# Kernel tuning notes

Hardware: AMD Instinct MI355X
Metric: run time of the kernel (lower is better)

## Reference

```python
import jax, jax.numpy as jnp
import numpy as np

T, B, I, H = 100, 64, 256, 512


def setup_inputs() -> dict:
    key = jax.random.key(0)
    ks = jax.random.split(key, 7)
    # torch kaiming_uniform_(a=sqrt(5)) + fan_in bias init -> uniform(-1/sqrt(fan_in), 1/sqrt(fan_in))
    b_ih = 1.0 / np.sqrt(I)
    b_hh = 1.0 / np.sqrt(H)
    return {
        "input": jax.random.normal(ks[0], (T, B, I), jnp.float32),
        "initial_h": jax.random.normal(ks[1], (B, H), jnp.float32),
        "initial_c": jax.random.normal(ks[2], (B, H), jnp.float32),
        "weight_ih": jax.random.uniform(ks[3], (4 * H, I), jnp.float32, -b_ih, b_ih),
        "weight_hh": jax.random.uniform(ks[4], (4 * H, H), jnp.float32, -b_hh, b_hh),
        "bias_ih": jax.random.uniform(ks[5], (4 * H,), jnp.float32, -b_ih, b_ih),
        "bias_hh": jax.random.uniform(ks[6], (4 * H,), jnp.float32, -b_hh, b_hh),
    }


def reference(input, initial_h, initial_c, weight_ih, weight_hh, bias_ih, bias_hh):
    Bsz, Isz = input.shape[1], input.shape[2]
    Hs = initial_h.shape[1]

    def step(carry, x_t):
        hx, cx, ev_ih, ev_hh, ev_b = carry
        # standard LSTM gates, torch gate order: i, f, g, o
        gates = x_t @ weight_ih.T + hx @ weight_hh.T + bias_ih + bias_hh  # [B,4H]
        i_g, f_g, g_g, o_g = jnp.split(gates, 4, axis=1)
        i = jax.nn.sigmoid(i_g)
        f = jax.nn.sigmoid(f_g)
        g = jnp.tanh(g_g)
        o = jax.nn.sigmoid(o_g)
        cy = f * cx + i * g
        hy = o * jnp.tanh(cy)
        # e-prop instantaneous derivatives of c_t wrt the i/f/g pre-activations
        d_i = g * i * (1.0 - i)          # [B,H]
        d_f = cx * f * (1.0 - f)
        d_g = i * (1.0 - g * g)
        d = jnp.concatenate([d_i, d_f, d_g], axis=1)[:, :, None]  # [B,3H,1]
        f3 = jnp.tile(f, (1, 3))[:, :, None]                      # [B,3H,1]
        # eligibility-trace recursion: ev_t = f_t * ev_{t-1} + d_t (outer) input
        ev_ih = f3 * ev_ih + d * x_t[:, None, :]   # [B,3H,I]
        ev_hh = f3 * ev_hh + d * hx[:, None, :]    # [B,3H,H]
        ev_b = f3 * ev_b + d                       # [B,3H,1]
        return (hy, cy, ev_ih, ev_hh, ev_b), hy

    ev_ih0 = jnp.zeros((Bsz, 3 * Hs, Isz), input.dtype)
    ev_hh0 = jnp.zeros((Bsz, 3 * Hs, Hs), input.dtype)
    ev_b0 = jnp.zeros((Bsz, 3 * Hs, 1), input.dtype)
    (hx, cx, ev_ih, ev_hh, ev_b), outputs = jax.lax.scan(
        step, (initial_h, initial_c, ev_ih0, ev_hh0, ev_b0), input
    )
    return outputs, cx, ev_ih, ev_hh, ev_b
```

## Files before the change

### kernel.cpp

```cpp
#include <hip/hip_runtime.h>
#include <math.h>

#define TT 100
#define BB 64
#define II 256
#define HH 512
#define G4H 2048
#define G3H 1536

#define OFF_GT    0
#define OFF_HBUF  13107200
#define OFF_FBUF  16416768
#define OFF_DBUF  19693568
#define OFF_CT    29523968
#define OFF_XT    29556736
#define OFF_WIHT  31195136
#define OFF_WHHT  31719424

#define O_OUT   0
#define O_CX    3276800
#define O_EVIH  3309568
#define O_EVHH  28475392
#define O_EVB   78807040

__global__ __launch_bounds__(256) void tp64(const float* __restrict__ src,
                                            float* __restrict__ dst,
                                            int R, int C,
                                            long sstride, long dstride) {
  __shared__ float tile[64][65];
  src += (long)blockIdx.z * sstride;
  dst += (long)blockIdx.z * dstride;
  int r0 = blockIdx.y * 64, c0 = blockIdx.x * 64;
  int tx = threadIdx.x & 15, tq = threadIdx.x >> 4;
#pragma unroll
  for (int p = 0; p < 4; ++p) {
    int rl = p * 16 + tq;
    float4 v = *(const float4*)(src + (long)(r0 + rl) * C + c0 + tx * 4);
    tile[rl][tx * 4 + 0] = v.x; tile[rl][tx * 4 + 1] = v.y;
    tile[rl][tx * 4 + 2] = v.z; tile[rl][tx * 4 + 3] = v.w;
  }
  __syncthreads();
#pragma unroll
  for (int p = 0; p < 4; ++p) {
    int cl = p * 16 + tq;
    float4 v;
    v.x = tile[tx * 4 + 0][cl]; v.y = tile[tx * 4 + 1][cl];
    v.z = tile[tx * 4 + 2][cl]; v.w = tile[tx * 4 + 3][cl];
    *(float4*)(dst + (long)(c0 + cl) * R + r0 + tx * 4) = v;
  }
}

__global__ __launch_bounds__(256) void make_whhg(const float* __restrict__ WhhT,
                                                 float* __restrict__ WhhG) {
  int gid = blockIdx.x * 256 + threadIdx.x;
  int k = gid >> 11, j = gid & 2047;
  float v = WhhT[gid];
  WhhG[(long)k * G4H + ((j & 511) << 2) + (j >> 9)] = v;
}

template <int BK, int KTILES, bool BIAS, bool ZSHIFT>
__global__ __launch_bounds__(256) void gemm_tn(
    const float* __restrict__ A, long batchA, int lda,
    const float* __restrict__ Z, long batchZ, int ldz,
    const float* __restrict__ Z0, long batchZ0,
    float* __restrict__ C, long batchC, int ldc,
    const float* __restrict__ bia, const float* __restrict__ bib) {
  __shared__ float As[BK][64];
  __shared__ float Zs[BK][64];
  int tid = threadIdx.x;
  int tn = tid & 15, tm = tid >> 4;
  int m0 = blockIdx.x * 64, n0 = blockIdx.y * 64;
  long bz = blockIdx.z;
  const float* Ab = A + bz * batchA + m0;
  const float* Zb = Z + bz * batchZ + n0;
  const float* Z0b = ZSHIFT ? (Z0 + bz * batchZ0 + n0) : nullptr;
  float acc[4][4] = {};
  for (int kt = 0; kt < KTILES; ++kt) {
    int k0 = kt * BK;
#pragma unroll
    for (int p = tid; p < BK * 64; p += 256) {
      int r = p >> 6, c = p & 63;
      int k = k0 + r;
      As[r][c] = Ab[(long)k * lda + c];
      const float* zr;
      if (ZSHIFT)
        zr = (k == 0) ? Z0b : (Zb + (long)(k - 1) * ldz);
      else
        zr = Zb + (long)k * ldz;
      Zs[r][c] = zr[c];
    }
    __syncthreads();
#pragma unroll 4
    for (int kk = 0; kk < BK; ++kk) {
      float4 a = *(const float4*)&As[kk][tm * 4];
      float4 z = *(const float4*)&Zs[kk][tn * 4];
      float av[4] = {a.x, a.y, a.z, a.w};
      float zv[4] = {z.x, z.y, z.z, z.w};
#pragma unroll
      for (int q = 0; q < 4; ++q)
#pragma unroll
        for (int r = 0; r < 4; ++r)
          acc[q][r] = fmaf(av[q], zv[r], acc[q][r]);
    }
    __syncthreads();
  }
  float* Cb = C + bz * batchC + n0 + tn * 4;
#pragma unroll
  for (int q = 0; q < 4; ++q) {
    int m = m0 + tm * 4 + q;
    float bv = BIAS ? (bia[m] + bib[m]) : 0.f;
    float4 v;
    v.x = acc[q][0] + bv; v.y = acc[q][1] + bv;
    v.z = acc[q][2] + bv; v.w = acc[q][3] + bv;
    *(float4*)(Cb + (long)m * ldc) = v;
  }
}

__global__ __launch_bounds__(512) void lstm_step2(const float* __restrict__ G_T,
                                                  const float* __restrict__ WhhG,
                                                  float* __restrict__ Hbuf,
                                                  float* __restrict__ cT,
                                                  float* __restrict__ Fbuf,
                                                  float* __restrict__ Dbuf,
                                                  int t) {
  __shared__ float red[2][4][4][64];
  int tid = threadIdx.x;
  int lane = tid & 63;
  int wave = __builtin_amdgcn_readfirstlane(tid >> 6);
  int hl = wave & 1, kp = wave >> 1;
  int hh = blockIdx.x * 2 + hl;
  float a0 = 0.f, a1 = 0.f, a2 = 0.f, a3 = 0.f;
  const float* hp = Hbuf + (long)t * (HH * BB) + kp * 128 * BB + lane;
  const float* wp = WhhG + (long)(kp * 128) * G4H + hh * 4;
#pragma unroll 4
  for (int k = 0; k < 128; ++k) {
    float h = hp[(long)k * BB];
    float4 w = *(const float4*)(wp + (long)k * G4H);
    a0 = fmaf(w.x, h, a0);
    a1 = fmaf(w.y, h, a1);
    a2 = fmaf(w.z, h, a2);
    a3 = fmaf(w.w, h, a3);
  }
  red[hl][kp][0][lane] = a0;
  red[hl][kp][1][lane] = a1;
  red[hl][kp][2][lane] = a2;
  red[hl][kp][3][lane] = a3;
  __syncthreads();
  if (tid < 128) {
    int b = tid & 63, h2 = tid >> 6;
    int hhx = blockIdx.x * 2 + h2;
    const float* gp = G_T + (long)t * (G4H * BB) + hhx * BB + b;
    float g[4];
#pragma unroll
    for (int q = 0; q < 4; ++q)
      g[q] = gp[(long)q * (HH * BB)] + red[h2][0][q][b] + red[h2][1][q][b] +
             red[h2][2][q][b] + red[h2][3][q][b];
    float ig = 1.f / (1.f + expf(-g[0]));
    float fg = 1.f / (1.f + expf(-g[1]));
    float gg = tanhf(g[2]);
    float og = 1.f / (1.f + expf(-g[3]));
    int idx = hhx * BB + b;
    float co = cT[idx];
    float cy = fg * co + ig * gg;
    cT[idx] = cy;
    Hbuf[(long)(t + 1) * (HH * BB) + idx] = og * tanhf(cy);
    Fbuf[(long)t * (HH * BB) + idx] = fg;
    float* dp = Dbuf + (long)t * (G3H * BB) + idx;
    dp[0] = gg * ig * (1.f - ig);
    dp[HH * BB] = co * fg * (1.f - fg);
    dp[2 * HH * BB] = ig * (1.f - gg * gg);
  }
}

__global__ __launch_bounds__(256) void suffix_scale(float* __restrict__ Dbuf,
                                                    const float* __restrict__ Fbuf,
                                                    float* __restrict__ evb) {
  int g = blockIdx.x * 256 + threadIdx.x;
  int b = g & 63, hh = g >> 6;
  float P = 1.f, e0 = 0.f, e1 = 0.f, e2 = 0.f;
#pragma unroll 2
  for (int t = TT - 1; t >= 0; --t) {
    float* dp = Dbuf + (long)t * (G3H * BB) + hh * BB + b;
    float v0 = dp[0] * P, v1 = dp[HH * BB] * P, v2 = dp[2 * HH * BB] * P;
    dp[0] = v0; dp[HH * BB] = v1; dp[2 * HH * BB] = v2;
    e0 += v0; e1 += v1; e2 += v2;
    P *= Fbuf[(long)t * (HH * BB) + hh * BB + b];
  }
  evb[b * G3H + hh] = e0;
  evb[b * G3H + HH + hh] = e1;
  evb[b * G3H + 2 * HH + hh] = e2;
}

extern "C" void kernel_launch(void* const* d_in, const int* in_sizes, int n_in,
                              void* d_out, int out_size, void* d_ws, size_t ws_size,
                              hipStream_t stream) {
  const float* x   = (const float*)d_in[0];
  const float* h0  = (const float*)d_in[1];
  const float* c0  = (const float*)d_in[2];
  const float* Wih = (const float*)d_in[3];
  const float* Whh = (const float*)d_in[4];
  const float* bih = (const float*)d_in[5];
  const float* bhh = (const float*)d_in[6];
  float* out = (float*)d_out;
  float* ws = (float*)d_ws;

  float* G_T   = ws + OFF_GT;
  float* DbufT = ws + OFF_GT;
  float* Hbuf  = ws + OFF_HBUF;
  float* Fbuf  = ws + OFF_FBUF;
  float* Dbuf  = ws + OFF_DBUF;
  float* cT    = ws + OFF_CT;
  float* xT    = ws + OFF_XT;
  float* WhhG  = ws + OFF_XT;
  float* WihT  = ws + OFF_WIHT;
  float* WhhT  = ws + OFF_WHHT;

  tp64<<<dim3(II / 64, G4H / 64, 1), 256, 0, stream>>>(Wih, WihT, G4H, II, 0, 0);
  tp64<<<dim3(HH / 64, G4H / 64, 1), 256, 0, stream>>>(Whh, WhhT, G4H, HH, 0, 0);
  tp64<<<dim3(II / 64, 1, TT), 256, 0, stream>>>(x, xT, BB, II, BB * II, BB * II);
  tp64<<<dim3(HH / 64, 1, 1), 256, 0, stream>>>(h0, Hbuf, BB, HH, 0, 0);
  tp64<<<dim3(HH / 64, 1, 1), 256, 0, stream>>>(c0, cT, BB, HH, 0, 0);

  gemm_tn<64, 4, true, false><<<dim3(G4H / 64, 1, TT), 256, 0, stream>>>(
      WihT, 0, G4H, xT, (long)II * BB, BB, nullptr, 0,
      G_T, (long)G4H * BB, BB, bih, bhh);

  make_whhg<<<dim3(HH * G4H / 256, 1, 1), 256, 0, stream>>>(WhhT, WhhG);

  for (int t = 0; t < TT; ++t) {
    lstm_step2<<<dim3(HH / 2, 1, 1), 512, 0, stream>>>(G_T, WhhG, Hbuf, cT,
                                                       Fbuf, Dbuf, t);
  }

  suffix_scale<<<dim3(HH * BB / 256, 1, 1), 256, 0, stream>>>(Dbuf, Fbuf,
                                                              out + O_EVB);

  tp64<<<dim3(1, TT * G3H / 64, 1), 256, 0, stream>>>(Dbuf, DbufT, TT * G3H, BB,
                                                      0, 0);

  tp64<<<dim3(1, HH / 64, TT), 256, 0, stream>>>(Hbuf + HH * BB, out + O_OUT,
                                                 HH, BB, HH * BB, HH * BB);
  tp64<<<dim3(1, HH / 64, 1), 256, 0, stream>>>(cT, out + O_CX, HH, BB, 0, 0);

  gemm_tn<20, 5, false, false><<<dim3(G3H / 64, II / 64, BB), 256, 0, stream>>>(
      DbufT, (long)TT * G3H, G3H, x, (long)II, (long)BB * II, nullptr, 0,
      out + O_EVIH, (long)G3H * II, II, nullptr, nullptr);

  gemm_tn<20, 5, false, true><<<dim3(G3H / 64, HH / 64, BB), 256, 0, stream>>>(
      DbufT, (long)TT * G3H, G3H, out + O_OUT, (long)HH, (long)BB * HH,
      h0, (long)HH,
      out + O_EVHH, (long)G3H * HH, HH, nullptr, nullptr);
}
```

Before: 1.778 ms.

## Fuse LSTM time loop into one persistent cooperative kernel with grid barrier

Replaces the 100 per-timestep kernel launches with a single cooperative persistent kernel of 256 blocks that loops over time, synchronizing via per-block flag counters in global memory (acquire/release atomics, polling). Each block now owns 2 hidden units across all 8 K-slices, keeps the cell state in registers, and prefetches the next step's input-gate preactivations while it waits at the barrier. This removes kernel launch and drain overhead at every step. In exchange, correctness depends on all blocks being co-resident, and the spin barrier adds polling traffic.

```diff
diff --git a/kernel.cpp b/kernel.cpp
--- a/kernel.cpp
+++ b/kernel.cpp
@@ -7,6 +7,7 @@
 #define HH 512
 #define G4H 2048
 #define G3H 1536
+#define NBLK 256
 
 #define OFF_GT    0
 #define OFF_HBUF  13107200
@@ -51,8 +52,10 @@
 }
 
 __global__ __launch_bounds__(256) void make_whhg(const float* __restrict__ WhhT,
-                                                 float* __restrict__ WhhG) {
+                                                 float* __restrict__ WhhG,
+                                                 int* __restrict__ bar) {
   int gid = blockIdx.x * 256 + threadIdx.x;
+  if (gid < NBLK) bar[gid] = 0;
   int k = gid >> 11, j = gid & 2047;
   float v = WhhT[gid];
   WhhG[(long)k * G4H + ((j & 511) << 2) + (j >> 9)] = v;
@@ -116,60 +119,109 @@
   }
 }
 
-__global__ __launch_bounds__(512) void lstm_step2(const float* __restrict__ G_T,
-                                                  const float* __restrict__ WhhG,
-                                                  float* __restrict__ Hbuf,
-                                                  float* __restrict__ cT,
-                                                  float* __restrict__ Fbuf,
-                                                  float* __restrict__ Dbuf,
-                                                  int t) {
-  __shared__ float red[2][4][4][64];
+__global__ __launch_bounds__(512, 4) void lstm_rec(
+    const float* __restrict__ G_T, const float* __restrict__ WhhG,
+    float* __restrict__ Hbuf, float* __restrict__ cT,
+    float* __restrict__ Fbuf, float* __restrict__ Dbuf,
+    int* __restrict__ bar) {
+  __shared__ float red[8][8][64];
   int tid = threadIdx.x;
   int lane = tid & 63;
   int wave = __builtin_amdgcn_readfirstlane(tid >> 6);
-  int hl = wave & 1, kp = wave >> 1;
-  int hh = blockIdx.x * 2 + hl;
-  float a0 = 0.f, a1 = 0.f, a2 = 0.f, a3 = 0.f;
-  const float* hp = Hbuf + (long)t * (HH * BB) + kp * 128 * BB + lane;
-  const float* wp = WhhG + (long)(kp * 128) * G4H + hh * 4;
+  int bx = blockIdx.x;
+  const float* wp = WhhG + (long)(wave * 64) * G4H + bx * 8;
+  int h2 = tid >> 6;
+  int b = tid & 63;
+  float creg = 0.f;
+  if (tid < 128) creg = cT[(bx * 2 + h2) * BB + b];
+
+  float gpre0 = 0.f, gpre1 = 0.f, gpre2 = 0.f, gpre3 = 0.f;
+  if (tid < 128) {
+    const float* gp = G_T + (bx * 2 + h2) * BB + b;
+    gpre0 = gp[0l * HH * BB];
+    gpre1 = gp[1l * HH * BB];
+    gpre2 = gp[2l * HH * BB];
+    gpre3 = gp[3l * HH * BB];
+  }
+
+  for (int t = 0; t < TT; ++t) {
+    const float* hp = Hbuf + (long)t * (HH * BB) + (wave * 64) * BB + lane;
+    float a0 = 0.f, a1 = 0.f, a2 = 0.f, a3 = 0.f;
+    float a4 = 0.f, a5 = 0.f, a6 = 0.f, a7 = 0.f;
 #pragma unroll 4
-  for (int k = 0; k < 128; ++k) {
-    float h = hp[(long)k * BB];
-    float4 w = *(const float4*)(wp + (long)k * G4H);
-    a0 = fmaf(w.x, h, a0);
-    a1 = fmaf(w.y, h, a1);
-    a2 = fmaf(w.z, h, a2);
-    a3 = fmaf(w.w, h, a3);
-  }
-  red[hl][kp][0][lane] = a0;
-  red[hl][kp][1][lane] = a1;
-  red[hl][kp][2][lane] = a2;
-  red[hl][kp][3][lane] = a3;
-  __syncthreads();
-  if (tid < 128) {
-    int b = tid & 63, h2 = tid >> 6;
-    int hhx = blockIdx.x * 2 + h2;
-    const float* gp = G_T + (long)t * (G4H * BB) + hhx * BB + b;
-    float g[4];
-#pragma unroll
-    for (int q = 0; q < 4; ++q)
-      g[q] = gp[(long)q * (HH * BB)] + red[h2][0][q][b] + red[h2][1][q][b] +
-             red[h2][2][q][b] + red[h2][3][q][b];
-    float ig = 1.f / (1.f + expf(-g[0]));
-    float fg = 1.f / (1.f + expf(-g[1]));
-    float gg = tanhf(g[2]);
-    float og = 1.f / (1.f + expf(-g[3]));
-    int idx = hhx * BB + b;
-    float co = cT[idx];
-    float cy = fg * co + ig * gg;
-    cT[idx] = cy;
-    Hbuf[(long)(t + 1) * (HH * BB) + idx] = og * tanhf(cy);
-    Fbuf[(long)t * (HH * BB) + idx] = fg;
-    float* dp = Dbuf + (long)t * (G3H * BB) + idx;
-    dp[0] = gg * ig * (1.f - ig);
-    dp[HH * BB] = co * fg * (1.f - fg);
-    dp[2 * HH * BB] = ig * (1.f - gg * gg);
-  }
+    for (int k = 0; k < 64; ++k) {
+      float h = hp[(long)k * BB];
+      float4 w0 = *(const float4*)(wp + (long)k * G4H);
+      float4 w1 = *(const float4*)(wp + (long)k * G4H + 4);
+      a0 = fmaf(w0.x, h, a0); a1 = fmaf(w0.y, h, a1);
+      a2 = fmaf(w0.z, h, a2); a3 = fmaf(w0.w, h, a3);
+      a4 = fmaf(w1.x, h, a4); a5 = fmaf(w1.y, h, a5);
+      a6 = fmaf(w1.z, h, a6); a7 = fmaf(w1.w, h, a7);
+    }
+    red[wave][0][lane] = a0; red[wave][1][lane] = a1;
+    red[wave][2][lane] = a2; red[wave][3][lane] = a3;
+    red[wave][4][lane] = a4; red[wave][5][lane] = a5;
+    red[wave][6][lane] = a6; red[wave][7][lane] = a7;
+    __syncthreads();
+    if (tid < 128) {
+      float g0 = gpre0, g1 = gpre1, g2 = gpre2, g3 = gpre3;
+#pragma unroll
+      for (int kp = 0; kp < 8; ++kp) {
+        g0 += red[kp][h2 * 4 + 0][b];
+        g1 += red[kp][h2 * 4 + 1][b];
+        g2 += red[kp][h2 * 4 + 2][b];
+        g3 += red[kp][h2 * 4 + 3][b];
+      }
+      float ig = 1.f / (1.f + expf(-g0));
+      float fg = 1.f / (1.f + expf(-g1));
+      float gg = tanhf(g2);
+      float og = 1.f / (1.f + expf(-g3));
+      int idx = (bx * 2 + h2) * BB + b;
+      float co = creg;
+      float cy = fg * co + ig * gg;
+      creg = cy;
+      Hbuf[(long)(t + 1) * (HH * BB) + idx] = og * tanhf(cy);
+      Fbuf[(long)t * (HH * BB) + idx] = fg;
+      float* dp = Dbuf + (long)t * (G3H * BB) + idx;
+      dp[0] = gg * ig * (1.f - ig);
+      dp[HH * BB] = co * fg * (1.f - fg);
+      dp[2 * HH * BB] = ig * (1.f - gg * gg);
+    }
+    __syncthreads();
+    if (t < TT - 1) {
+      if (tid == 0)
+        __hip_atomic_store(&bar[bx], t + 1, __ATOMIC_RELEASE,
+                           __HIP_MEMORY_SCOPE_AGENT);
+      if (tid < 128) {
+        const float* gp =
+            G_T + (long)(t + 1) * (G4H * BB) + (bx * 2 + h2) * BB + b;
+        gpre0 = gp[0l * HH * BB];
+        gpre1 = gp[1l * HH * BB];
+        gpre2 = gp[2l * HH * BB];
+        gpre3 = gp[3l * HH * BB];
+      }
+      if (tid < 64) {
+        int tgt = t + 1;
+        bool ok;
+        do {
+          int v0 = __hip_atomic_load(&bar[lane], __ATOMIC_RELAXED,
+                                     __HIP_MEMORY_SCOPE_AGENT);
+          int v1 = __hip_atomic_load(&bar[lane + 64], __ATOMIC_RELAXED,
+                                     __HIP_MEMORY_SCOPE_AGENT);
+          int v2 = __hip_atomic_load(&bar[lane + 128], __ATOMIC_RELAXED,
+                                     __HIP_MEMORY_SCOPE_AGENT);
+          int v3 = __hip_atomic_load(&bar[lane + 192], __ATOMIC_RELAXED,
+                                     __HIP_MEMORY_SCOPE_AGENT);
+          ok = (v0 >= tgt) && (v1 >= tgt) && (v2 >= tgt) && (v3 >= tgt);
+          if (!__all(ok)) __builtin_amdgcn_s_sleep(1);
+          else break;
+        } while (true);
+        __builtin_amdgcn_fence(__ATOMIC_ACQUIRE, "agent");
+      }
+      __syncthreads();
+    }
+  }
+  if (tid < 128) cT[(bx * 2 + h2) * BB + b] = creg;
 }
 
 __global__ __launch_bounds__(256) void suffix_scale(float* __restrict__ Dbuf,
@@ -213,6 +265,7 @@
   float* xT    = ws + OFF_XT;
   float* WhhG  = ws + OFF_XT;
   float* WihT  = ws + OFF_WIHT;
+  int*   bar   = (int*)(ws + OFF_WIHT);
   float* WhhT  = ws + OFF_WHHT;
 
   tp64<<<dim3(II / 64, G4H / 64, 1), 256, 0, stream>>>(Wih, WihT, G4H, II, 0, 0);
@@ -225,11 +278,20 @@
       WihT, 0, G4H, xT, (long)II * BB, BB, nullptr, 0,
       G_T, (long)G4H * BB, BB, bih, bhh);
 
-  make_whhg<<<dim3(HH * G4H / 256, 1, 1), 256, 0, stream>>>(WhhT, WhhG);
-
-  for (int t = 0; t < TT; ++t) {
-    lstm_step2<<<dim3(HH / 2, 1, 1), 512, 0, stream>>>(G_T, WhhG, Hbuf, cT,
-                                                       Fbuf, Dbuf, t);
+  make_whhg<<<dim3(HH * G4H / 256, 1, 1), 256, 0, stream>>>(WhhT, WhhG, bar);
+
+  {
+    const float* a_gt = G_T;
+    const float* a_wg = WhhG;
+    float* a_hb = Hbuf;
+    float* a_ct = cT;
+    float* a_fb = Fbuf;
+    float* a_db = Dbuf;
+    int* a_bar = bar;
+    void* args[] = {(void*)&a_gt, (void*)&a_wg, (void*)&a_hb, (void*)&a_ct,
+                    (void*)&a_fb, (void*)&a_db, (void*)&a_bar};
+    hipLaunchCooperativeKernel((const void*)lstm_rec, dim3(NBLK), dim3(512),
+                               args, 0, stream);
   }
 
   suffix_scale<<<dim3(HH * BB / 256, 1, 1), 256, 0, stream>>>(Dbuf, Fbuf,
```

Result: slower. 2.238 ms (+25.8%).
